# Kernel optimization log

Hardware: AMD Instinct MI355X
Metric: run time of the kernel (lower is better)

## Reference

```python
import jax, jax.numpy as jnp
import numpy as np

N = 100000      # nodes
E = 1600000     # edges (avg degree 16)
D_IN, D_H, D_OUT = 128, 128, 64


def setup_inputs() -> dict:
    key = jax.random.key(0)
    ks = jax.random.split(key, 8)
    x = jax.random.normal(ks[0], (N, D_IN), dtype=jnp.float32)
    edge_index = jax.random.randint(ks[1], (2, E), 0, N, dtype=jnp.int64)

    def lin(k, fi, fo):
        s = float(1.0 / np.sqrt(fi))
        return jax.random.normal(k, (fi, fo), dtype=jnp.float32) * s

    return {
        "x": x,
        "edge_index": edge_index,
        "W0": lin(ks[2], D_IN, D_H),  "b0": jnp.zeros((D_H,), jnp.float32),
        "W1": lin(ks[3], D_H, D_H),   "b1": jnp.zeros((D_H,), jnp.float32),
        "W2": lin(ks[4], D_H, D_OUT), "b2": jnp.zeros((D_OUT,), jnp.float32),
    }


def gcn_conv(x, W, b, src, dst, deg_inv_sqrt):
    # PyG GCNConv: h = x W; out = D^-1/2 (A + I) D^-1/2 h + b
    h = x @ W                                             # [N, F_out]
    coef = deg_inv_sqrt[src] * deg_inv_sqrt[dst]          # [E]
    msg = h[src] * coef[:, None]                          # [E, F_out] gather
    out = jax.ops.segment_sum(msg, dst, num_segments=N)   # scatter-add
    out = out + (deg_inv_sqrt * deg_inv_sqrt)[:, None] * h  # self-loops
    return out + b


def reference(x, edge_index, W0, b0, W1, b1, W2, b2):
    src, dst = edge_index[0], edge_index[1]
    # degree includes the self-loop (+1), matching add_self_loops fill_value=1
    deg = jnp.zeros((N,), x.dtype).at[dst].add(1.0) + 1.0
    dis = jax.lax.rsqrt(deg)

    h = jax.nn.relu(gcn_conv(x, W0, b0, src, dst, dis))   # dropout: eval mode -> identity
    h = jax.nn.relu(gcn_conv(h, W1, b1, src, dst, dis))
    h = gcn_conv(h, W2, b2, src, dst, dis)
    return jax.nn.log_softmax(h, axis=1)
```

## Files before the change

kernel.cpp:

```cpp
#include <hip/hip_runtime.h>
#include <cstddef>

#define NN 100000
#define NE 1600000
#define CB_SH 9
#define NCB ((NN + 511) >> CB_SH)
#define BIN_D 32
#define CAP 8960
#define SORT_D CAP
#define SC_BLOCKS 768

typedef unsigned int uint;
typedef unsigned short ushort;
typedef short bf16x8 __attribute__((ext_vector_type(8)));
typedef float f32x16 __attribute__((ext_vector_type(16)));

__device__ inline uint bf16_rne(float f) {
  uint u = __float_as_uint(f);
  u += 0x7fffu + ((u >> 16) & 1u);
  return u >> 16;
}
__device__ inline float blo(uint u) { return __uint_as_float(u << 16); }
__device__ inline float bhi(uint u) { return __uint_as_float(u & 0xffff0000u); }

__global__ void __launch_bounds__(256) k_init(int* __restrict__ gcur) {
  int i = threadIdx.x;
  if (i < NCB) gcur[i] = i * CAP;
}

__global__ void __launch_bounds__(256) k_binA(const int* __restrict__ src,
                                              const int* __restrict__ dst,
                                              int* __restrict__ gcur,
                                              uint* __restrict__ ebuf, int E) {
  __shared__ uint bins[NCB][BIN_D + 1];
  __shared__ uint bcnt[NCB];
  int t = threadIdx.x;
  for (int j = t; j < NCB; j += 256) bcnt[j] = 0;
  const int per = (E + SC_BLOCKS - 1) / SC_BLOCKS;
  int e0 = blockIdx.x * per, e1 = min(E, e0 + per);
  __syncthreads();
  for (int rb = e0; rb < e1; rb += 2048) {
    #pragma unroll
    for (int r = 0; r < 8; ++r) {
      int i = rb + r * 256 + t;
      if (i < e1) {
        uint s = (uint)src[i], d = (uint)dst[i];
        uint b = d >> CB_SH;
        uint rec = s | ((d & 511u) << 17);
        uint slot = atomicAdd(&bcnt[b], 1u);
        if (slot < BIN_D) bins[b][slot] = rec;
        else ebuf[atomicAdd(&gcur[b], 1)] = rec;
      }
    }
    __syncthreads();
    if (t < NCB) {
      uint c = bcnt[t]; if (c > BIN_D) c = BIN_D;
      if (c) {
        int base = atomicAdd(&gcur[t], (int)c);
        for (uint i = 0; i < c; ++i) ebuf[base + i] = bins[t][i];
      }
      bcnt[t] = 0;
    }
    __syncthreads();
  }
}

__global__ void __launch_bounds__(512) k_bcnt(const uint* __restrict__ ebuf,
                                              const int* __restrict__ gcur,
                                              int* __restrict__ row_ptr,
                                              float* __restrict__ dis, int N, int E) {
  __shared__ uint c[512];
  __shared__ uint wsum[8];
  int b = blockIdx.x, t = threadIdx.x, lane = t & 63, wv = t >> 6;
  c[t] = 0;

  uint v = (t < NCB && t < b) ? (uint)(gcur[t] - t * CAP) : 0u;
  #pragma unroll
  for (int d = 32; d; d >>= 1) v += __shfl_xor(v, d, 64);
  if (lane == 0) wsum[wv] = v;
  __syncthreads();
  uint ebase = 0;
  #pragma unroll
  for (int j = 0; j < 8; ++j) ebase += wsum[j];

  int cntb = gcur[b] - b * CAP;
  const uint* __restrict__ eb = ebuf + (size_t)b * CAP;
  int i = t;
  for (; i + 3 * 512 < cntb; i += 4 * 512) {
    uint r0 = eb[i], r1 = eb[i + 512], r2 = eb[i + 1024], r3 = eb[i + 1536];
    atomicAdd(&c[r0 >> 17], 1u);
    atomicAdd(&c[r1 >> 17], 1u);
    atomicAdd(&c[r2 >> 17], 1u);
    atomicAdd(&c[r3 >> 17], 1u);
  }
  for (; i < cntb; i += 512)
    atomicAdd(&c[eb[i] >> 17], 1u);
  __syncthreads();

  uint deg = c[t];
  uint x = deg;
  #pragma unroll
  for (int d = 1; d < 64; d <<= 1) {
    uint y = __shfl_up(x, (uint)d, 64);
    if (lane >= d) x += y;
  }
  if (lane == 63) wsum[wv] = x;
  __syncthreads();
  uint wexcl = 0;
  for (int j = 0; j < wv; ++j) wexcl += wsum[j];
  uint excl = ebase + wexcl + (x - deg);

  int g = (b << CB_SH) + t;
  if (g < N) {
    row_ptr[g] = (int)excl;
    dis[g] = rsqrtf((float)deg + 1.0f);
  }
  if (b == 0 && t == 0) row_ptr[N] = E;
}

__global__ void __launch_bounds__(512) k_sortB(const uint* __restrict__ ebuf,
                                               const int* __restrict__ gcur,
                                               const int* __restrict__ row_ptr,
                                               const float* __restrict__ dis,
                                               uint* __restrict__ edges, int N) {
  __shared__ uint sbuf[SORT_D];
  __shared__ int lcur[512];
  __shared__ float disl[512];
  int b = blockIdx.x, t = threadIdx.x;
  int node0 = b << CB_SH;
  int ebase = row_ptr[node0];
  int g = node0 + t;
  lcur[t] = (g < N) ? (row_ptr[g] - ebase) : 0;
  disl[t] = (g < N) ? dis[g] : 0.f;
  __syncthreads();
  int cntb = gcur[b] - b * CAP;
  const uint* __restrict__ eb = ebuf + (size_t)b * CAP;
  int i = t;
  for (; i + 3 * 512 < cntb; i += 4 * 512) {
    uint rec[4]; float ds[4];
    #pragma unroll
    for (int j = 0; j < 4; ++j) rec[j] = eb[i + j * 512];
    #pragma unroll
    for (int j = 0; j < 4; ++j) ds[j] = dis[rec[j] & 0x1ffffu];
    #pragma unroll
    for (int j = 0; j < 4; ++j) {
      uint dl = rec[j] >> 17;
      uint orec = (bf16_rne(ds[j] * disl[dl]) << 17) | (rec[j] & 0x1ffffu);
      int pos = atomicAdd(&lcur[dl], 1);
      if (pos < SORT_D) sbuf[pos] = orec;
      else edges[ebase + pos] = orec;
    }
  }
  for (; i < cntb; i += 512) {
    uint rec = eb[i];
    uint dl = rec >> 17;
    uint orec = (bf16_rne(dis[rec & 0x1ffffu] * disl[dl]) << 17) | (rec & 0x1ffffu);
    int pos = atomicAdd(&lcur[dl], 1);
    if (pos < SORT_D) sbuf[pos] = orec;
    else edges[ebase + pos] = orec;
  }
  __syncthreads();
  int lim = min(cntb, SORT_D);
  for (int j = t; j < lim; j += 512)
    edges[ebase + j] = sbuf[j];
}

template <int FOUT, bool BF16IN>
__global__ void __launch_bounds__(256) k_gemm(const void* __restrict__ Xv,
                                              const float* __restrict__ W,
                                              ushort* __restrict__ Hb, int M) {
  constexpr int NCT = FOUT / 32;
  constexpr int TPW = NCT / 2;
  __shared__ alignas(16) ushort Af[2 * 8 * 64 * 8];
  __shared__ alignas(16) ushort Wf[NCT * 8 * 64 * 8];
  int t = threadIdx.x, lane = t & 63, wv = t >> 6;
  int m0 = blockIdx.x * 64;

  {
    int m = t >> 2;
    int gm = m0 + m;
    int rb = m >> 5, ml = m & 31;
    #pragma unroll
    for (int i = 0; i < 4; ++i) {
      int g = (t & 3) + i * 4;
      uint4 p = make_uint4(0u, 0u, 0u, 0u);
      if (gm < M) {
        if (BF16IN) {
          const ushort* X = (const ushort*)Xv;
          p = *reinterpret_cast<const uint4*>(X + (size_t)gm * 128 + g * 8);
        } else {
          const float* X = (const float*)Xv;
          float4 va = *reinterpret_cast<const float4*>(X + (size_t)gm * 128 + g * 8);
          float4 vb = *reinterpret_cast<const float4*>(X + (size_t)gm * 128 + g * 8 + 4);
          p.x = bf16_rne(va.x) | (bf16_rne(va.y) << 16);
          p.y = bf16_rne(va.z) | (bf16_rne(va.w) << 16);
          p.z = bf16_rne(vb.x) | (bf16_rne(vb.y) << 16);
          p.w = bf16_rne(vb.z) | (bf16_rne(vb.w) << 16);
        }
      }
      int kc = g >> 1, khi = g & 1;
      int ln = khi * 32 + ml;
      *reinterpret_cast<uint4*>(&Af[(((rb * 8 + kc) * 64) + ln) * 8]) = p;
    }
  }
  {
    constexpr int ITERS = 128 * FOUT / 4 / 256;
    #pragma unroll
    for (int it = 0; it < ITERS; ++it) {
      int lin = it * 256 + t;
      int k = lin / (FOUT / 4);
      int n = (lin % (FOUT / 4)) * 4;
      float4 vw = *reinterpret_cast<const float4*>(W + (size_t)k * FOUT + n);
      int kc = k >> 4, khi = (k >> 3) & 1, j = k & 7;
      float arr[4] = {vw.x, vw.y, vw.z, vw.w};
      #pragma unroll
      for (int e = 0; e < 4; ++e) {
        int nn = n + e;
        int c = nn >> 5;
        int ln = khi * 32 + (nn & 31);
        Wf[(((c * 8 + kc) * 64) + ln) * 8 + j] = (ushort)bf16_rne(arr[e]);
      }
    }
  }
  __syncthreads();

  f32x16 acc[TPW];
  #pragma unroll
  for (int tp = 0; tp < TPW; ++tp)
    #pragma unroll
    for (int r = 0; r < 16; ++r) acc[tp][r] = 0.f;

  int rb = wv & 1, cg = wv >> 1;
  #pragma unroll
  for (int kc = 0; kc < 8; ++kc) {
    bf16x8 a = *reinterpret_cast<bf16x8*>(&Af[((rb * 8 + kc) * 64 + lane) * 8]);
    #pragma unroll
    for (int tp = 0; tp < TPW; ++tp) {
      int c = cg * TPW + tp;
      bf16x8 bb = *reinterpret_cast<bf16x8*>(&Wf[((c * 8 + kc) * 64 + lane) * 8]);
      acc[tp] = __builtin_amdgcn_mfma_f32_32x32x16_bf16(a, bb, acc[tp], 0, 0, 0);
    }
  }

  #pragma unroll
  for (int tp = 0; tp < TPW; ++tp) {
    int col = (cg * TPW + tp) * 32 + (lane & 31);
    #pragma unroll
    for (int reg = 0; reg < 16; ++reg) {
      int row = m0 + rb * 32 + 4 * (lane >> 5) + (reg & 3) + 8 * (reg >> 2);
      if (row < M) Hb[(size_t)row * FOUT + col] = (ushort)bf16_rne(acc[tp][reg]);
    }
  }
}

__global__ void __launch_bounds__(256) k_agg128(const uint* __restrict__ hb,
                                                const int* __restrict__ row_ptr,
                                                const uint* __restrict__ edges,
                                                const float* __restrict__ dis,
                                                const float* __restrict__ bias,
                                                uint* __restrict__ outb, int N) {
  int t = threadIdx.x;
  int lane = t & 63, wv = t >> 6;
  int hw = lane >> 5;
  int hbase = lane & 32;
  int sl = lane & 15;
  int grp = (lane >> 4) & 1;
  int n = blockIdx.x * 8 + wv * 2 + hw;
  if (n >= N) return;
  const uint4* __restrict__ h4 = reinterpret_cast<const uint4*>(hb);
  int beg = row_ptr[n], end = row_ptr[n + 1];

  float acc[8];
  #pragma unroll
  for (int k = 0; k < 8; ++k) acc[k] = 0.f;

  int p = beg;
  for (; p + 16 <= end; p += 16) {
    uint r = edges[p + sl];
    #pragma unroll
    for (int s = 0; s < 8; ++s) {
      uint rec = __shfl(r, hbase + s * 2 + grp, 64);
      uint4 v = h4[(size_t)(rec & 0x1ffffu) * 16 + sl];
      float c = __uint_as_float((rec >> 17) << 16);
      acc[0] = fmaf(blo(v.x), c, acc[0]);
      acc[1] = fmaf(bhi(v.x), c, acc[1]);
      acc[2] = fmaf(blo(v.y), c, acc[2]);
      acc[3] = fmaf(bhi(v.y), c, acc[3]);
      acc[4] = fmaf(blo(v.z), c, acc[4]);
      acc[5] = fmaf(bhi(v.z), c, acc[5]);
      acc[6] = fmaf(blo(v.w), c, acc[6]);
      acc[7] = fmaf(bhi(v.w), c, acc[7]);
    }
  }
  if (p < end) {
    int idx = p + sl;
    uint r = (idx < end) ? edges[idx] : 0u;
    #pragma unroll
    for (int s = 0; s < 8; ++s) {
      int e = s * 2 + grp;
      uint rec = __shfl(r, hbase + e, 64);
      if (p + e < end) {
        uint4 v = h4[(size_t)(rec & 0x1ffffu) * 16 + sl];
        float c = __uint_as_float((rec >> 17) << 16);
        acc[0] = fmaf(blo(v.x), c, acc[0]);
        acc[1] = fmaf(bhi(v.x), c, acc[1]);
        acc[2] = fmaf(blo(v.y), c, acc[2]);
        acc[3] = fmaf(bhi(v.y), c, acc[3]);
        acc[4] = fmaf(blo(v.z), c, acc[4]);
        acc[5] = fmaf(bhi(v.z), c, acc[5]);
        acc[6] = fmaf(blo(v.w), c, acc[6]);
        acc[7] = fmaf(bhi(v.w), c, acc[7]);
      }
    }
  }
  #pragma unroll
  for (int k = 0; k < 8; ++k) acc[k] += __shfl_xor(acc[k], 16, 64);

  float dn = dis[n], sc = dn * dn;
  if (!(lane & 16)) {
    uint4 hv = h4[(size_t)n * 16 + sl];
    const float4* b4 = reinterpret_cast<const float4*>(bias);
    float4 ba = b4[sl * 2], bb2 = b4[sl * 2 + 1];
    float o0 = fmaxf(fmaf(sc, blo(hv.x), acc[0]) + ba.x, 0.f);
    float o1 = fmaxf(fmaf(sc, bhi(hv.x), acc[1]) + ba.y, 0.f);
    float o2 = fmaxf(fmaf(sc, blo(hv.y), acc[2]) + ba.z, 0.f);
    float o3 = fmaxf(fmaf(sc, bhi(hv.y), acc[3]) + ba.w, 0.f);
    float o4 = fmaxf(fmaf(sc, blo(hv.z), acc[4]) + bb2.x, 0.f);
    float o5 = fmaxf(fmaf(sc, bhi(hv.z), acc[5]) + bb2.y, 0.f);
    float o6 = fmaxf(fmaf(sc, blo(hv.w), acc[6]) + bb2.z, 0.f);
    float o7 = fmaxf(fmaf(sc, bhi(hv.w), acc[7]) + bb2.w, 0.f);
    uint4 pb;
    pb.x = bf16_rne(o0) | (bf16_rne(o1) << 16);
    pb.y = bf16_rne(o2) | (bf16_rne(o3) << 16);
    pb.z = bf16_rne(o4) | (bf16_rne(o5) << 16);
    pb.w = bf16_rne(o6) | (bf16_rne(o7) << 16);
    reinterpret_cast<uint4*>(outb)[(size_t)n * 16 + sl] = pb;
  }
}

__global__ void __launch_bounds__(256) k_agg64(const uint* __restrict__ hb,
                                               const int* __restrict__ row_ptr,
                                               const uint* __restrict__ edges,
                                               const float* __restrict__ dis,
                                               const float* __restrict__ bias,
                                               float* __restrict__ out, int N) {
  int t = threadIdx.x;
  int lane = t & 63, wv = t >> 6;
  int hw = lane >> 5;
  int hbase = lane & 32;
  int sl = lane & 7;
  int grp = (lane >> 3) & 3;
  int rl = lane & 15;
  int n = blockIdx.x * 8 + wv * 2 + hw;
  if (n >= N) return;
  const uint4* __restrict__ h4 = reinterpret_cast<const uint4*>(hb);
  int beg = row_ptr[n], end = row_ptr[n + 1];

  float acc[8];
  #pragma unroll
  for (int k = 0; k < 8; ++k) acc[k] = 0.f;

  int p = beg;
  for (; p + 16 <= end; p += 16) {
    uint r = edges[p + rl];
    #pragma unroll
    for (int s = 0; s < 4; ++s) {
      uint rec = __shfl(r, hbase + s * 4 + grp, 64);
      uint4 v = h4[(size_t)(rec & 0x1ffffu) * 8 + sl];
      float c = __uint_as_float((rec >> 17) << 16);
      acc[0] = fmaf(blo(v.x), c, acc[0]);
      acc[1] = fmaf(bhi(v.x), c, acc[1]);
      acc[2] = fmaf(blo(v.y), c, acc[2]);
      acc[3] = fmaf(bhi(v.y), c, acc[3]);
      acc[4] = fmaf(blo(v.z), c, acc[4]);
      acc[5] = fmaf(bhi(v.z), c, acc[5]);
      acc[6] = fmaf(blo(v.w), c, acc[6]);
      acc[7] = fmaf(bhi(v.w), c, acc[7]);
    }
  }
  if (p < end) {
    int idx = p + rl;
    uint r = (idx < end) ? edges[idx] : 0u;
    #pragma unroll
    for (int s = 0; s < 4; ++s) {
      int e = s * 4 + grp;
      uint rec = __shfl(r, hbase + e, 64);
      if (p + e < end) {
        uint4 v = h4[(size_t)(rec & 0x1ffffu) * 8 + sl];
        float c = __uint_as_float((rec >> 17) << 16);
        acc[0] = fmaf(blo(v.x), c, acc[0]);
        acc[1] = fmaf(bhi(v.x), c, acc[1]);
        acc[2] = fmaf(blo(v.y), c, acc[2]);
        acc[3] = fmaf(bhi(v.y), c, acc[3]);
        acc[4] = fmaf(blo(v.z), c, acc[4]);
        acc[5] = fmaf(bhi(v.z), c, acc[5]);
        acc[6] = fmaf(blo(v.w), c, acc[6]);
        acc[7] = fmaf(bhi(v.w), c, acc[7]);
      }
    }
  }
  #pragma unroll
  for (int k = 0; k < 8; ++k) {
    acc[k] += __shfl_xor(acc[k], 8, 64);
    acc[k] += __shfl_xor(acc[k], 16, 64);
  }

  float dn = dis[n];
  uint4 hv = h4[(size_t)n * 8 + sl];
  const float4* b4 = reinterpret_cast<const float4*>(bias);
  float4 ba = b4[sl * 2], bb2 = b4[sl * 2 + 1];
  float z[8];
  z[0] = fmaf(dn * dn, blo(hv.x), acc[0]) + ba.x;
  z[1] = fmaf(dn * dn, bhi(hv.x), acc[1]) + ba.y;
  z[2] = fmaf(dn * dn, blo(hv.y), acc[2]) + ba.z;
  z[3] = fmaf(dn * dn, bhi(hv.y), acc[3]) + ba.w;
  z[4] = fmaf(dn * dn, blo(hv.z), acc[4]) + bb2.x;
  z[5] = fmaf(dn * dn, bhi(hv.z), acc[5]) + bb2.y;
  z[6] = fmaf(dn * dn, blo(hv.w), acc[6]) + bb2.z;
  z[7] = fmaf(dn * dn, bhi(hv.w), acc[7]) + bb2.w;

  float m = z[0];
  #pragma unroll
  for (int k = 1; k < 8; ++k) m = fmaxf(m, z[k]);
  m = fmaxf(m, __shfl_xor(m, 1, 64));
  m = fmaxf(m, __shfl_xor(m, 2, 64));
  m = fmaxf(m, __shfl_xor(m, 4, 64));
  float e = 0.f;
  #pragma unroll
  for (int k = 0; k < 8; ++k) e += __expf(z[k] - m);
  e += __shfl_xor(e, 1, 64);
  e += __shfl_xor(e, 2, 64);
  e += __shfl_xor(e, 4, 64);
  float lse = m + __logf(e);

  if ((lane & 31) < 8) {
    float4* orow = reinterpret_cast<float4*>(out + (size_t)n * 64);
    orow[sl * 2]     = make_float4(z[0] - lse, z[1] - lse, z[2] - lse, z[3] - lse);
    orow[sl * 2 + 1] = make_float4(z[4] - lse, z[5] - lse, z[6] - lse, z[7] - lse);
  }
}

extern "C" void kernel_launch(void* const* d_in, const int* in_sizes, int n_in,
                              void* d_out, int out_size, void* d_ws, size_t ws_size,
                              hipStream_t stream) {
  const float* x  = (const float*)d_in[0];
  const int*   ei = (const int*)d_in[1];
  const float* W0 = (const float*)d_in[2];
  const float* b0 = (const float*)d_in[3];
  const float* W1 = (const float*)d_in[4];
  const float* b1 = (const float*)d_in[5];
  const float* W2 = (const float*)d_in[6];
  const float* b2 = (const float*)d_in[7];
  float* out = (float*)d_out;

  const int N = NN, E = NE;
  const int* src = ei;
  const int* dst = ei + E;

  char* ws = (char*)d_ws;
  size_t off = 0;
  auto alloc = [&](size_t bytes) -> void* {
    off = (off + 255) & ~(size_t)255;
    void* p = ws + off;
    off += bytes;
    return p;
  };
  float*  dis     = (float*)alloc((size_t)N * 4);
  int*    row_ptr = (int*)alloc((size_t)(N + 1) * 4);
  int*    gcur    = (int*)alloc((size_t)NCB * 4);
  uint*   ebuf    = (uint*)alloc((size_t)NCB * CAP * 4);
  uint*   edges   = (uint*)alloc((size_t)E * 4);
  ushort* bufAb   = (ushort*)alloc((size_t)N * 128 * 2);
  ushort* bufBb   = (ushort*)alloc((size_t)N * 128 * 2);

  k_init<<<1, 256, 0, stream>>>(gcur);
  k_binA<<<SC_BLOCKS, 256, 0, stream>>>(src, dst, gcur, ebuf, E);
  k_bcnt<<<NCB, 512, 0, stream>>>(ebuf, gcur, row_ptr, dis, N, E);
  k_sortB<<<NCB, 512, 0, stream>>>(ebuf, gcur, row_ptr, dis, edges, N);

  const int gemm_grid = (N + 63) / 64;
  const int node_grid = (N + 7) / 8;

  k_gemm<128, false><<<gemm_grid, 256, 0, stream>>>(x, W0, bufAb, N);
  k_agg128<<<node_grid, 256, 0, stream>>>((const uint*)bufAb, row_ptr, edges, dis, b0, (uint*)bufBb, N);
  k_gemm<128, true><<<gemm_grid, 256, 0, stream>>>(bufBb, W1, bufAb, N);
  k_agg128<<<node_grid, 256, 0, stream>>>((const uint*)bufAb, row_ptr, edges, dis, b1, (uint*)bufBb, N);
  k_gemm<64, true><<<gemm_grid, 256, 0, stream>>>(bufBb, W2, bufAb, N);
  k_agg64<<<node_grid, 256, 0, stream>>>((const uint*)bufAb, row_ptr, edges, dis, b2, out, N);
}
```

Baseline: 386.5 us.

## Fold source-degree normalization into GEMM epilogue and sort each node's edges by source

The GEMM epilogue now scales each output row by its node's inverse-sqrt degree. Aggregation therefore becomes a plain sum of gathered rows, scaled once by the destination's factor, with the self-loop term folded into that same scale. This drops the per-edge coefficient computation and bf16 packing in the sort kernel and the per-edge multiply in aggregation. Each node's neighbour list is also insertion-sorted by source index in LDS to improve gather locality, and the aggregation loops issue all row loads before accumulating. The trade-offs are the extra insertion-sort work, the removal of the LDS-overflow fallback path, and slightly different bf16 rounding from pre-scaling.

```diff
diff --git a/kernel.cpp b/kernel.cpp
--- a/kernel.cpp
+++ b/kernel.cpp
@@ -121,61 +121,66 @@
 __global__ void __launch_bounds__(512) k_sortB(const uint* __restrict__ ebuf,
                                                const int* __restrict__ gcur,
                                                const int* __restrict__ row_ptr,
-                                               const float* __restrict__ dis,
                                                uint* __restrict__ edges, int N) {
   __shared__ uint sbuf[SORT_D];
   __shared__ int lcur[512];
-  __shared__ float disl[512];
+  __shared__ int sst[512];
   int b = blockIdx.x, t = threadIdx.x;
   int node0 = b << CB_SH;
   int ebase = row_ptr[node0];
   int g = node0 + t;
-  lcur[t] = (g < N) ? (row_ptr[g] - ebase) : 0;
-  disl[t] = (g < N) ? dis[g] : 0.f;
+  int st = (g < N) ? (row_ptr[g] - ebase) : 0;
+  lcur[t] = st;
+  sst[t] = st;
   __syncthreads();
   int cntb = gcur[b] - b * CAP;
   const uint* __restrict__ eb = ebuf + (size_t)b * CAP;
   int i = t;
   for (; i + 3 * 512 < cntb; i += 4 * 512) {
-    uint rec[4]; float ds[4];
+    uint rec[4];
     #pragma unroll
     for (int j = 0; j < 4; ++j) rec[j] = eb[i + j * 512];
     #pragma unroll
-    for (int j = 0; j < 4; ++j) ds[j] = dis[rec[j] & 0x1ffffu];
-    #pragma unroll
     for (int j = 0; j < 4; ++j) {
-      uint dl = rec[j] >> 17;
-      uint orec = (bf16_rne(ds[j] * disl[dl]) << 17) | (rec[j] & 0x1ffffu);
-      int pos = atomicAdd(&lcur[dl], 1);
-      if (pos < SORT_D) sbuf[pos] = orec;
-      else edges[ebase + pos] = orec;
+      int pos = atomicAdd(&lcur[rec[j] >> 17], 1);
+      sbuf[pos] = rec[j] & 0x1ffffu;
     }
   }
   for (; i < cntb; i += 512) {
     uint rec = eb[i];
-    uint dl = rec >> 17;
-    uint orec = (bf16_rne(dis[rec & 0x1ffffu] * disl[dl]) << 17) | (rec & 0x1ffffu);
-    int pos = atomicAdd(&lcur[dl], 1);
-    if (pos < SORT_D) sbuf[pos] = orec;
-    else edges[ebase + pos] = orec;
-  }
-  __syncthreads();
-  int lim = min(cntb, SORT_D);
-  for (int j = t; j < lim; j += 512)
+    int pos = atomicAdd(&lcur[rec >> 17], 1);
+    sbuf[pos] = rec & 0x1ffffu;
+  }
+  __syncthreads();
+  int en = lcur[t];
+  for (int ii = st + 1; ii < en; ++ii) {
+    uint key = sbuf[ii];
+    int j = ii - 1;
+    while (j >= st && sbuf[j] > key) { sbuf[j + 1] = sbuf[j]; --j; }
+    sbuf[j + 1] = key;
+  }
+  __syncthreads();
+  for (int j = t; j < cntb; j += 512)
     edges[ebase + j] = sbuf[j];
 }
 
 template <int FOUT, bool BF16IN>
 __global__ void __launch_bounds__(256) k_gemm(const void* __restrict__ Xv,
                                               const float* __restrict__ W,
+                                              const float* __restrict__ dis,
                                               ushort* __restrict__ Hb, int M) {
   constexpr int NCT = FOUT / 32;
   constexpr int TPW = NCT / 2;
   __shared__ alignas(16) ushort Af[2 * 8 * 64 * 8];
   __shared__ alignas(16) ushort Wf[NCT * 8 * 64 * 8];
+  __shared__ float diss[64];
   int t = threadIdx.x, lane = t & 63, wv = t >> 6;
   int m0 = blockIdx.x * 64;
 
+  if (t < 64) {
+    int gm = m0 + t;
+    diss[t] = (gm < M) ? dis[gm] : 0.f;
+  }
   {
     int m = t >> 2;
     int gm = m0 + m;
@@ -247,8 +252,9 @@
     int col = (cg * TPW + tp) * 32 + (lane & 31);
     #pragma unroll
     for (int reg = 0; reg < 16; ++reg) {
-      int row = m0 + rb * 32 + 4 * (lane >> 5) + (reg & 3) + 8 * (reg >> 2);
-      if (row < M) Hb[(size_t)row * FOUT + col] = (ushort)bf16_rne(acc[tp][reg]);
+      int lr = rb * 32 + 4 * (lane >> 5) + (reg & 3) + 8 * (reg >> 2);
+      int row = m0 + lr;
+      if (row < M) Hb[(size_t)row * FOUT + col] = (ushort)bf16_rne(acc[tp][reg] * diss[lr]);
     }
   }
 }
@@ -277,19 +283,22 @@
   int p = beg;
   for (; p + 16 <= end; p += 16) {
     uint r = edges[p + sl];
+    uint rec[8];
+    #pragma unroll
+    for (int s = 0; s < 8; ++s) rec[s] = __shfl(r, hbase + s * 2 + grp, 64);
+    uint4 v[8];
+    #pragma unroll
+    for (int s = 0; s < 8; ++s) v[s] = h4[(size_t)rec[s] * 16 + sl];
     #pragma unroll
     for (int s = 0; s < 8; ++s) {
-      uint rec = __shfl(r, hbase + s * 2 + grp, 64);
-      uint4 v = h4[(size_t)(rec & 0x1ffffu) * 16 + sl];
-      float c = __uint_as_float((rec >> 17) << 16);
-      acc[0] = fmaf(blo(v.x), c, acc[0]);
-      acc[1] = fmaf(bhi(v.x), c, acc[1]);
-      acc[2] = fmaf(blo(v.y), c, acc[2]);
-      acc[3] = fmaf(bhi(v.y), c, acc[3]);
-      acc[4] = fmaf(blo(v.z), c, acc[4]);
-      acc[5] = fmaf(bhi(v.z), c, acc[5]);
-      acc[6] = fmaf(blo(v.w), c, acc[6]);
-      acc[7] = fmaf(bhi(v.w), c, acc[7]);
+      acc[0] += blo(v[s].x);
+      acc[1] += bhi(v[s].x);
+      acc[2] += blo(v[s].y);
+      acc[3] += bhi(v[s].y);
+      acc[4] += blo(v[s].z);
+      acc[5] += bhi(v[s].z);
+      acc[6] += blo(v[s].w);
+      acc[7] += bhi(v[s].w);
     }
   }
   if (p < end) {
@@ -300,35 +309,34 @@
       int e = s * 2 + grp;
       uint rec = __shfl(r, hbase + e, 64);
       if (p + e < end) {
-        uint4 v = h4[(size_t)(rec & 0x1ffffu) * 16 + sl];
-        float c = __uint_as_float((rec >> 17) << 16);
-        acc[0] = fmaf(blo(v.x), c, acc[0]);
-        acc[1] = fmaf(bhi(v.x), c, acc[1]);
-        acc[2] = fmaf(blo(v.y), c, acc[2]);
-        acc[3] = fmaf(bhi(v.y), c, acc[3]);
-        acc[4] = fmaf(blo(v.z), c, acc[4]);
-        acc[5] = fmaf(bhi(v.z), c, acc[5]);
-        acc[6] = fmaf(blo(v.w), c, acc[6]);
-        acc[7] = fmaf(bhi(v.w), c, acc[7]);
+        uint4 v = h4[(size_t)rec * 16 + sl];
+        acc[0] += blo(v.x);
+        acc[1] += bhi(v.x);
+        acc[2] += blo(v.y);
+        acc[3] += bhi(v.y);
+        acc[4] += blo(v.z);
+        acc[5] += bhi(v.z);
+        acc[6] += blo(v.w);
+        acc[7] += bhi(v.w);
       }
     }
   }
   #pragma unroll
   for (int k = 0; k < 8; ++k) acc[k] += __shfl_xor(acc[k], 16, 64);
 
-  float dn = dis[n], sc = dn * dn;
+  float dn = dis[n];
   if (!(lane & 16)) {
     uint4 hv = h4[(size_t)n * 16 + sl];
     const float4* b4 = reinterpret_cast<const float4*>(bias);
     float4 ba = b4[sl * 2], bb2 = b4[sl * 2 + 1];
-    float o0 = fmaxf(fmaf(sc, blo(hv.x), acc[0]) + ba.x, 0.f);
-    float o1 = fmaxf(fmaf(sc, bhi(hv.x), acc[1]) + ba.y, 0.f);
-    float o2 = fmaxf(fmaf(sc, blo(hv.y), acc[2]) + ba.z, 0.f);
-    float o3 = fmaxf(fmaf(sc, bhi(hv.y), acc[3]) + ba.w, 0.f);
-    float o4 = fmaxf(fmaf(sc, blo(hv.z), acc[4]) + bb2.x, 0.f);
-    float o5 = fmaxf(fmaf(sc, bhi(hv.z), acc[5]) + bb2.y, 0.f);
-    float o6 = fmaxf(fmaf(sc, blo(hv.w), acc[6]) + bb2.z, 0.f);
-    float o7 = fmaxf(fmaf(sc, bhi(hv.w), acc[7]) + bb2.w, 0.f);
+    float o0 = fmaxf((acc[0] + blo(hv.x)) * dn + ba.x, 0.f);
+    float o1 = fmaxf((acc[1] + bhi(hv.x)) * dn + ba.y, 0.f);
+    float o2 = fmaxf((acc[2] + blo(hv.y)) * dn + ba.z, 0.f);
+    float o3 = fmaxf((acc[3] + bhi(hv.y)) * dn + ba.w, 0.f);
+    float o4 = fmaxf((acc[4] + blo(hv.z)) * dn + bb2.x, 0.f);
+    float o5 = fmaxf((acc[5] + bhi(hv.z)) * dn + bb2.y, 0.f);
+    float o6 = fmaxf((acc[6] + blo(hv.w)) * dn + bb2.z, 0.f);
+    float o7 = fmaxf((acc[7] + bhi(hv.w)) * dn + bb2.w, 0.f);
     uint4 pb;
     pb.x = bf16_rne(o0) | (bf16_rne(o1) << 16);
     pb.y = bf16_rne(o2) | (bf16_rne(o3) << 16);
@@ -363,19 +371,22 @@
   int p = beg;
   for (; p + 16 <= end; p += 16) {
     uint r = edges[p + rl];
+    uint rec[4];
+    #pragma unroll
+    for (int s = 0; s < 4; ++s) rec[s] = __shfl(r, hbase + s * 4 + grp, 64);
+    uint4 v[4];
+    #pragma unroll
+    for (int s = 0; s < 4; ++s) v[s] = h4[(size_t)rec[s] * 8 + sl];
     #pragma unroll
     for (int s = 0; s < 4; ++s) {
-      uint rec = __shfl(r, hbase + s * 4 + grp, 64);
-      uint4 v = h4[(size_t)(rec & 0x1ffffu) * 8 + sl];
-      float c = __uint_as_float((rec >> 17) << 16);
-      acc[0] = fmaf(blo(v.x), c, acc[0]);
-      acc[1] = fmaf(bhi(v.x), c, acc[1]);
-      acc[2] = fmaf(blo(v.y), c, acc[2]);
-      acc[3] = fmaf(bhi(v.y), c, acc[3]);
-      acc[4] = fmaf(blo(v.z), c, acc[4]);
-      acc[5] = fmaf(bhi(v.z), c, acc[5]);
-      acc[6] = fmaf(blo(v.w), c, acc[6]);
-      acc[7] = fmaf(bhi(v.w), c, acc[7]);
+      acc[0] += blo(v[s].x);
+      acc[1] += bhi(v[s].x);
+      acc[2] += blo(v[s].y);
+      acc[3] += bhi(v[s].y);
+      acc[4] += blo(v[s].z);
+      acc[5] += bhi(v[s].z);
+      acc[6] += blo(v[s].w);
+      acc[7] += bhi(v[s].w);
     }
   }
   if (p < end) {
@@ -386,16 +397,15 @@
       int e = s * 4 + grp;
       uint rec = __shfl(r, hbase + e, 64);
       if (p + e < end) {
-        uint4 v = h4[(size_t)(rec & 0x1ffffu) * 8 + sl];
-        float c = __uint_as_float((rec >> 17) << 16);
-        acc[0] = fmaf(blo(v.x), c, acc[0]);
-        acc[1] = fmaf(bhi(v.x), c, acc[1]);
-        acc[2] = fmaf(blo(v.y), c, acc[2]);
-        acc[3] = fmaf(bhi(v.y), c, acc[3]);
-        acc[4] = fmaf(blo(v.z), c, acc[4]);
-        acc[5] = fmaf(bhi(v.z), c, acc[5]);
-        acc[6] = fmaf(blo(v.w), c, acc[6]);
-        acc[7] = fmaf(bhi(v.w), c, acc[7]);
+        uint4 v = h4[(size_t)rec * 8 + sl];
+        acc[0] += blo(v.x);
+        acc[1] += bhi(v.x);
+        acc[2] += blo(v.y);
+        acc[3] += bhi(v.y);
+        acc[4] += blo(v.z);
+        acc[5] += bhi(v.z);
+        acc[6] += blo(v.w);
+        acc[7] += bhi(v.w);
       }
     }
   }
@@ -410,14 +420,14 @@
   const float4* b4 = reinterpret_cast<const float4*>(bias);
   float4 ba = b4[sl * 2], bb2 = b4[sl * 2 + 1];
   float z[8];
-  z[0] = fmaf(dn * dn, blo(hv.x), acc[0]) + ba.x;
-  z[1] = fmaf(dn * dn, bhi(hv.x), acc[1]) + ba.y;
-  z[2] = fmaf(dn * dn, blo(hv.y), acc[2]) + ba.z;
-  z[3] = fmaf(dn * dn, bhi(hv.y), acc[3]) + ba.w;
-  z[4] = fmaf(dn * dn, blo(hv.z), acc[4]) + bb2.x;
-  z[5] = fmaf(dn * dn, bhi(hv.z), acc[5]) + bb2.y;
-  z[6] = fmaf(dn * dn, blo(hv.w), acc[6]) + bb2.z;
-  z[7] = fmaf(dn * dn, bhi(hv.w), acc[7]) + bb2.w;
+  z[0] = (acc[0] + blo(hv.x)) * dn + ba.x;
+  z[1] = (acc[1] + bhi(hv.x)) * dn + ba.y;
+  z[2] = (acc[2] + blo(hv.y)) * dn + ba.z;
+  z[3] = (acc[3] + bhi(hv.y)) * dn + ba.w;
+  z[4] = (acc[4] + blo(hv.z)) * dn + bb2.x;
+  z[5] = (acc[5] + bhi(hv.z)) * dn + bb2.y;
+  z[6] = (acc[6] + blo(hv.w)) * dn + bb2.z;
+  z[7] = (acc[7] + bhi(hv.w)) * dn + bb2.w;
 
   float m = z[0];
   #pragma unroll
@@ -476,15 +486,15 @@
   k_init<<<1, 256, 0, stream>>>(gcur);
   k_binA<<<SC_BLOCKS, 256, 0, stream>>>(src, dst, gcur, ebuf, E);
   k_bcnt<<<NCB, 512, 0, stream>>>(ebuf, gcur, row_ptr, dis, N, E);
-  k_sortB<<<NCB, 512, 0, stream>>>(ebuf, gcur, row_ptr, dis, edges, N);
+  k_sortB<<<NCB, 512, 0, stream>>>(ebuf, gcur, row_ptr, edges, N);
 
   const int gemm_grid = (N + 63) / 64;
   const int node_grid = (N + 7) / 8;
 
-  k_gemm<128, false><<<gemm_grid, 256, 0, stream>>>(x, W0, bufAb, N);
+  k_gemm<128, false><<<gemm_grid, 256, 0, stream>>>(x, W0, dis, bufAb, N);
   k_agg128<<<node_grid, 256, 0, stream>>>((const uint*)bufAb, row_ptr, edges, dis, b0, (uint*)bufBb, N);
-  k_gemm<128, true><<<gemm_grid, 256, 0, stream>>>(bufBb, W1, bufAb, N);
+  k_gemm<128, true><<<gemm_grid, 256, 0, stream>>>(bufBb, W1, dis, bufAb, N);
   k_agg128<<<node_grid, 256, 0, stream>>>((const uint*)bufAb, row_ptr, edges, dis, b1, (uint*)bufBb, N);
-  k_gemm<64, true><<<gemm_grid, 256, 0, stream>>>(bufBb, W2, bufAb, N);
+  k_gemm<64, true><<<gemm_grid, 256, 0, stream>>>(bufBb, W2, dis, bufAb, N);
   k_agg64<<<node_grid, 256, 0, stream>>>((const uint*)bufAb, row_ptr, edges, dis, b2, out, N);
 }
```

After: 439.5 us. 13.7% more time.
